# Optimization experiments

Measured on AMD Instinct MI355X. Metric: run time of the kernel, lower is better.

## Reference

```python
import jax, jax.numpy as jnp
import numpy as np

NUM_HEADS = 16
FIELD_SIZE = 512
SIGMA = 3.0
EMB = 1024


def _causal_kernel_fft(G, sigma):
    # kernel[i] = exp(-|i - G//2| / sigma) for i < G//2, else 0; normalized
    i = np.arange(G)
    dist = np.abs(i - G // 2)
    kernel = np.where(i >= G // 2, 0.0, np.exp(-dist / sigma)).astype(np.float32)
    kernel = kernel / (kernel.sum() + 1e-8)
    return jnp.asarray(np.fft.rfft(kernel), dtype=jnp.complex64)


def setup_inputs() -> dict:
    key = jax.random.key(0)
    ks = jax.random.split(key, 9)
    B, N, D = 4, 4096, EMB
    s = 1.0 / np.sqrt(D)
    return {
        "x": jax.random.normal(ks[0], (B, N, D), dtype=jnp.float32),
        "q_w": jax.random.uniform(ks[1], (D, D), minval=-s, maxval=s, dtype=jnp.float32),
        "q_b": jnp.zeros((D,), jnp.float32),
        "k_w": jax.random.uniform(ks[2], (D, D), minval=-s, maxval=s, dtype=jnp.float32),
        "k_b": jnp.zeros((D,), jnp.float32),
        "v_w": jax.random.uniform(ks[3], (D, D), minval=-s, maxval=s, dtype=jnp.float32),
        "v_b": jnp.zeros((D,), jnp.float32),
        "out_w": jax.random.uniform(ks[4], (D, D), minval=-s, maxval=s, dtype=jnp.float32),
        "out_b": jnp.zeros((D,), jnp.float32),
    }


def reference(x, q_w, q_b, k_w, k_b, v_w, v_b, out_w, out_b):
    B, N, D = x.shape
    H, hd, G = NUM_HEADS, D // NUM_HEADS, FIELD_SIZE

    # projections (q is computed in the original but unused downstream)
    q = x @ q_w.T + q_b  # noqa: F841 (faithful to original)
    k = (x @ k_w.T + k_b).reshape(B, N, H, hd).transpose(0, 2, 1, 3)  # (B,H,N,hd)
    v = (x @ v_w.T + v_b).reshape(B, N, H, hd).transpose(0, 2, 1, 3)

    # map sequence positions -> field bins (same for all b, h)
    pos = jnp.arange(N, dtype=jnp.float32) / max(N - 1, 1) * (G - 1)
    field_idx = jnp.clip(pos.astype(jnp.int32), 0, G - 1)  # (N,)

    # weighted values by key magnitude
    k_mag = jnp.linalg.norm(k, axis=-1, keepdims=True)  # (B,H,N,1)
    wv = v * k_mag  # (B,H,N,hd)

    # scatter-add tokens into field bins (vectorized over B,H,hd)
    field = jax.ops.segment_sum(wv.transpose(2, 0, 1, 3), field_idx,
                                num_segments=G)  # (G,B,H,hd)
    field = field.transpose(1, 2, 0, 3)  # (B,H,G,hd)

    # causal convolution along the field via FFT (circular, as in original)
    kfft = _causal_kernel_fft(G, SIGMA)
    f_fft = jnp.fft.rfft(field, n=G, axis=2)
    conv = jnp.fft.irfft(f_fft * kfft[None, None, :, None], n=G, axis=2)

    # gather back to token positions
    out = conv[:, :, field_idx, :]  # (B,H,N,hd)
    out = out.transpose(0, 2, 1, 3).reshape(B, N, D)
    return out @ out_w.T + out_b
```

## Files before the change

### kernel.cpp

```cpp
#include <hip/hip_runtime.h>
#include <hip/hip_bf16.h>

#define NPOS 4096
#define DIM  1024
#define GSZ  512

#define GAS __attribute__((address_space(1)))
#define LAS __attribute__((address_space(3)))

typedef __attribute__((ext_vector_type(8))) short bf16x8;
typedef __attribute__((ext_vector_type(4))) float f32x4;

__device__ __forceinline__ void async_load16(const void* g, void* l) {
  __builtin_amdgcn_global_load_lds((const GAS void*)g, (LAS void*)l, 16, 0, 0);
}

__device__ __forceinline__ int fidx_of(int n) {
  return (int)(((float)n / 4095.0f) * 511.0f);
}

__device__ __forceinline__ float bf2f(unsigned short s) {
  union { unsigned u; float f; } v; v.u = ((unsigned)s) << 16; return v.f;
}

__device__ __forceinline__ int bin_start(int g) {
  if (g >= GSZ) return NPOS;
  int i0 = (g * 4095 + 510) / 511;
  while (i0 > 0 && fidx_of(i0 - 1) >= g) --i0;
  while (i0 < NPOS && fidx_of(i0) < g) ++i0;
  return i0;
}

__device__ __forceinline__ void bin_range(int g, int& i0, int& i1) {
  i0 = bin_start(g);
  i1 = bin_start(g + 1);
}

__global__ __launch_bounds__(256) void cast_all(
    const float* __restrict__ x, const float* __restrict__ kw,
    const float* __restrict__ vw, const float* __restrict__ ow,
    __hip_bfloat16* __restrict__ xb, __hip_bfloat16* __restrict__ kvwb,
    __hip_bfloat16* __restrict__ outwb) {
  int blk = blockIdx.x;
  const float* src; __hip_bfloat16* dst; int off;
  if (blk < 8192)      { src = x;  dst = xb;              off = blk; }
  else if (blk < 8704) { src = kw; dst = kvwb;            off = blk - 8192; }
  else if (blk < 9216) { src = vw; dst = kvwb + 1048576;  off = blk - 8704; }
  else                 { src = ow; dst = outwb;           off = blk - 9216; }
  int i = (off * 256 + threadIdx.x) * 8;
  float4 f0 = *(const float4*)(src + i);
  float4 f1 = *(const float4*)(src + i + 4);
  ushort4 o0, o1;
  __hip_bfloat16 t;
  t = __float2bfloat16(f0.x); o0.x = *(unsigned short*)&t;
  t = __float2bfloat16(f0.y); o0.y = *(unsigned short*)&t;
  t = __float2bfloat16(f0.z); o0.z = *(unsigned short*)&t;
  t = __float2bfloat16(f0.w); o0.w = *(unsigned short*)&t;
  t = __float2bfloat16(f1.x); o1.x = *(unsigned short*)&t;
  t = __float2bfloat16(f1.y); o1.y = *(unsigned short*)&t;
  t = __float2bfloat16(f1.z); o1.z = *(unsigned short*)&t;
  t = __float2bfloat16(f1.w); o1.w = *(unsigned short*)&t;
  *(ushort4*)(dst + i) = o0;
  *(ushort4*)(dst + i + 4) = o1;
}


#define BAR()   __builtin_amdgcn_s_barrier()
#define LGKM0() do { asm volatile("s_waitcnt lgkmcnt(0)" ::: "memory"); \
                     __builtin_amdgcn_sched_barrier(0); } while (0)
#define VMW(N)  asm volatile("s_waitcnt vmcnt(" #N ")" ::: "memory")

#define STAGE_A(BUF, KT, C) \
  async_load16(ag0 + (size_t)(KT) * 64 + (size_t)(C) * 65536, &As[BUF][(C) * 4096 + ldst])
#define STAGE_B(BUF, KT, C) \
  async_load16(bg0 + (size_t)(KT) * 64 + (size_t)(C) * 65536, &Bs[BUF][(C) * 4096 + ldst])

#define STAGE_FULL(BUF, KT) do { \
    _Pragma("unroll") \
    for (int c_ = 0; c_ < 4; ++c_) { \
      STAGE_A(BUF, KT, c_); \
      STAGE_B(BUF, KT, c_); \
    } \
  } while (0)

#define LDA(BUF, MT, CB) (*(const bf16x8*)&As[BUF][abase + (MT) * 1024 + (CB)])
#define LDB(BUF, NT, CB) (*(const bf16x8*)&Bs[BUF][bbase + (NT) * 1024 + (CB)])

#define MFMA_Q(MQ, NQ, BF) do { \
    __builtin_amdgcn_s_setprio(1); \
    _Pragma("unroll") \
    for (int m_ = 0; m_ < 4; ++m_) { \
      _Pragma("unroll") \
      for (int n_ = 0; n_ < 2; ++n_) { \
        acc[(MQ)*4+m_][(NQ)*2+n_] = __builtin_amdgcn_mfma_f32_16x16x32_bf16( \
            af[m_][0], BF[n_][0], acc[(MQ)*4+m_][(NQ)*2+n_], 0, 0, 0); \
        acc[(MQ)*4+m_][(NQ)*2+n_] = __builtin_amdgcn_mfma_f32_16x16x32_bf16( \
            af[m_][1], BF[n_][1], acc[(MQ)*4+m_][(NQ)*2+n_], 0, 0, 0); \
      } \
    } \
    __builtin_amdgcn_s_setprio(0); \
  } while (0)

#define DO_TILE(BUF, KT) do { \
    const bool pf_ = (KT) + 2 < 16; \
     \
    _Pragma("unroll") \
    for (int m_ = 0; m_ < 4; ++m_) { af[m_][0] = LDA(BUF, m_, cb0); af[m_][1] = LDA(BUF, m_, cb1); } \
    _Pragma("unroll") \
    for (int n_ = 0; n_ < 2; ++n_) { b0f[n_][0] = LDB(BUF, n_, cb0); b0f[n_][1] = LDB(BUF, n_, cb1); } \
    BAR(); LGKM0(); \
    MFMA_Q(0, 0, b0f); \
    BAR(); \
     \
    _Pragma("unroll") \
    for (int n_ = 0; n_ < 2; ++n_) { b1f[n_][0] = LDB(BUF, 2 + n_, cb0); b1f[n_][1] = LDB(BUF, 2 + n_, cb1); } \
    if (pf_) { STAGE_A(BUF, (KT) + 2, 0); STAGE_A(BUF, (KT) + 2, 2); } \
    BAR(); LGKM0(); \
    MFMA_Q(0, 1, b1f); \
    BAR(); \
     \
    _Pragma("unroll") \
    for (int m_ = 0; m_ < 4; ++m_) { af[m_][0] = LDA(BUF, 4 + m_, cb0); af[m_][1] = LDA(BUF, 4 + m_, cb1); } \
    if (pf_) { STAGE_B(BUF, (KT) + 2, 0); STAGE_B(BUF, (KT) + 2, 1); \
               STAGE_B(BUF, (KT) + 2, 2); STAGE_B(BUF, (KT) + 2, 3); } \
    BAR(); LGKM0(); \
    MFMA_Q(1, 1, b1f); \
    BAR(); \
     \
    if (pf_) { STAGE_A(BUF, (KT) + 2, 1); STAGE_A(BUF, (KT) + 2, 3); } \
    MFMA_Q(1, 0, b0f); \
    if (pf_) { VMW(8); } else if ((KT) == 14) { VMW(0); } \
    BAR(); \
  } while (0)

__global__ __launch_bounds__(512, 2) void gemm_kv(
    const __hip_bfloat16* __restrict__ A,
    const __hip_bfloat16* __restrict__ B,
    const float* __restrict__ k_b, const float* __restrict__ v_b,
    __hip_bfloat16* __restrict__ Vb, float* __restrict__ knorm) {
  __shared__ __align__(16) __hip_bfloat16 As[2][16384];
  __shared__ __align__(16) __hip_bfloat16 Bs[2][16384];
  const int tid = threadIdx.x;

  const int l  = blockIdx.y * 64 + blockIdx.x;
  const int vv = (l & 7) * 64 + (l >> 3);
  const int bx = vv & 63, by = vv >> 6;
  const int bm = bx * 256;

  const int sb  = ((((tid & 7) * 16) ^ (((tid >> 3) & 7) << 4)) >> 1);
  const int r0  = tid >> 3;
  const __hip_bfloat16* ag0 = A + (size_t)(bm + r0) * 1024 + sb;
  const __hip_bfloat16* bg0 = B + (size_t)(by * 256 + r0) * 1024 + sb;
  const int ldst = tid * 8;

  const int wave = tid >> 6, lane = tid & 63;
  const int wr = wave >> 2, wc = wave & 3;
  const int m16 = lane & 15, quad = lane >> 4;
  const int swz  = (m16 & 7) << 4;
  const int cb0  = ((quad * 16)      ^ swz) >> 1;
  const int cb1  = ((quad * 16 + 64) ^ swz) >> 1;
  const int abase = wr * 8192 + m16 * 64;
  const int bbase = wc * 4096 + m16 * 64;

  f32x4 acc[8][4];
#pragma unroll
  for (int i = 0; i < 8; i++)
#pragma unroll
    for (int j2 = 0; j2 < 4; j2++) acc[i][j2] = (f32x4)0.f;

  bf16x8 af[4][2], b0f[2][2], b1f[2][2];

  STAGE_FULL(0, 0);
  STAGE_FULL(1, 1);
  VMW(8);
  BAR();

  for (int kt = 0; kt < 16; kt += 2) {
    DO_TILE(0, kt);
    DO_TILE(1, kt + 1);
  }

  if (by < 4) {
    const int head = by * 4 + wc;
    float bv[4];
#pragma unroll
    for (int nt = 0; nt < 4; nt++) bv[nt] = k_b[by * 256 + wc * 64 + nt * 16 + m16];
#pragma unroll
    for (int mt = 0; mt < 8; mt++) {
#pragma unroll
      for (int r = 0; r < 4; r++) {
        float s = 0.f;
#pragma unroll
        for (int nt = 0; nt < 4; nt++) {
          float t = acc[mt][nt][r] + bv[nt];
          s += t * t;
        }
        s += __shfl_xor(s, 1);
        s += __shfl_xor(s, 2);
        s += __shfl_xor(s, 4);
        s += __shfl_xor(s, 8);
        if (m16 == 0) {
          int row = bm + wr * 128 + mt * 16 + quad * 4 + r;
          knorm[(size_t)row * 16 + head] = sqrtf(s);
        }
      }
    }
  } else {
    const int colb = (by - 4) * 256 + wc * 64;
#pragma unroll
    for (int mt = 0; mt < 8; mt++) {
#pragma unroll
      for (int nt = 0; nt < 4; nt++) {
        int col = colb + nt * 16 + m16;
        float bvv = v_b[col];
#pragma unroll
        for (int r = 0; r < 4; r++) {
          int row = bm + wr * 128 + mt * 16 + quad * 4 + r;
          Vb[(size_t)row * 1024 + col] = __float2bfloat16(acc[mt][nt][r] + bvv);
        }
      }
    }
  }
}

__global__ __launch_bounds__(256) void gemm_outc(
    const __hip_bfloat16* __restrict__ A,
    const __hip_bfloat16* __restrict__ B,
    const float* __restrict__ bias,
    float* __restrict__ C) {
  const int K = 1024;
  __shared__ __align__(16) __hip_bfloat16 Aso[2][64 * 32];
  __shared__ __align__(16) __hip_bfloat16 Bso[2][64 * 32];
  __shared__ __align__(16) float ctile[64 * 68];
  const int tid = threadIdx.x;

  const int l   = blockIdx.y * 32 + blockIdx.x;
  const int xcd = l & 7, j = l >> 3;
  const int bx  = xcd * 4 + (j & 3);
  const int by  = j >> 2;
  const int bm = bx * 64, bn = by * 64;

  const int srow = tid >> 2;
  const int scol = (tid & 3) * 8;
  const __hip_bfloat16* ap = A + (size_t)(bm + srow) * K + scol;
  const __hip_bfloat16* bp = B + (size_t)(bn + srow) * K + scol;
  const int soff = srow * 32 + scol;

  const int wave = tid >> 6, lane = tid & 63;
  const int wm = (wave >> 1) * 32, wn = (wave & 1) * 32;
  const int m16 = lane & 15, quad = lane >> 4;

  f32x4 acc[2][2];
#pragma unroll
  for (int i = 0; i < 2; i++)
#pragma unroll
    for (int jj = 0; jj < 2; jj++) acc[i][jj] = (f32x4)0.f;

  for (int k0 = 0; k0 < K; k0 += 64) {
    async_load16(ap + k0,      &Aso[0][soff]);
    async_load16(bp + k0,      &Bso[0][soff]);
    async_load16(ap + k0 + 32, &Aso[1][soff]);
    async_load16(bp + k0 + 32, &Bso[1][soff]);
    __syncthreads();
#pragma unroll
    for (int h = 0; h < 2; h++) {
      bf16x8 afr[2], bfr[2];
#pragma unroll
      for (int mt = 0; mt < 2; mt++)
        afr[mt] = *(const bf16x8*)&Aso[h][(wm + mt * 16 + m16) * 32 + quad * 8];
#pragma unroll
      for (int nt = 0; nt < 2; nt++)
        bfr[nt] = *(const bf16x8*)&Bso[h][(wn + nt * 16 + m16) * 32 + quad * 8];
#pragma unroll
      for (int mt = 0; mt < 2; mt++)
#pragma unroll
        for (int nt = 0; nt < 2; nt++)
          acc[mt][nt] = __builtin_amdgcn_mfma_f32_16x16x32_bf16(afr[mt], bfr[nt], acc[mt][nt], 0, 0, 0);
    }
    __syncthreads();
  }

#pragma unroll
  for (int mt = 0; mt < 2; mt++) {
#pragma unroll
    for (int nt = 0; nt < 2; nt++) {
      int lcol = wn + nt * 16 + m16;
      float bv = bias[bn + lcol];
#pragma unroll
      for (int r = 0; r < 4; r++) {
        int lrow = wm + mt * 16 + quad * 4 + r;
        ctile[lrow * 68 + lcol] = acc[mt][nt][r] + bv;
      }
    }
  }
  __syncthreads();

  const int b  = bm >> 9;
  const int g0 = bm & (GSZ - 1);
  const int n0 = bin_start(g0);
  const int n1 = bin_start(g0 + 64);
  const int total = (n1 - n0) * 16;
  float* obase = C + (((size_t)b << 12)) * DIM + bn;
  for (int idx = tid; idx < total; idx += 256) {
    int n  = n0 + (idx >> 4);
    int c4 = (idx & 15) * 4;
    int lg = fidx_of(n) - g0;
    float4 v = *(const float4*)&ctile[lg * 68 + c4];
    *(float4*)(obase + (size_t)n * DIM + c4) = v;
  }
}

__global__ __launch_bounds__(256) void wv_field_kernel(
    const __hip_bfloat16* __restrict__ V, const float* __restrict__ knorm,
    float* __restrict__ field) {
  const int b = blockIdx.x, g = blockIdx.y;
  int i0, i1;
  bin_range(g, i0, i1);
  int cnt = i1 - i0;
  if (cnt > 9) cnt = 9;
  __shared__ float km[9][16];
  const int tid = threadIdx.x;
  if (tid < 144) {
    int r = tid >> 4, h = tid & 15;
    km[r][h] = (r < cnt) ? knorm[(size_t)(b * NPOS + i0 + r) * 16 + h] : 0.f;
  }
  __syncthreads();
  const int c0 = tid * 4, h = tid >> 4;
  const unsigned short* vbase = (const unsigned short*)V + (size_t)(b * NPOS + i0) * 1024 + c0;
  ushort4 vv[8];
  float ww[8];
#pragma unroll
  for (int j = 0; j < 8; ++j) {
    int jc = (j < cnt) ? j : 0;
    vv[j] = *(const ushort4*)(vbase + (size_t)jc * 1024);
    ww[j] = (j < cnt) ? km[j][h] : 0.f;
  }
  float a0 = 0.f, a1 = 0.f, a2 = 0.f, a3 = 0.f;
#pragma unroll
  for (int j = 0; j < 8; ++j) {
    a0 += ww[j] * bf2f(vv[j].x); a1 += ww[j] * bf2f(vv[j].y);
    a2 += ww[j] * bf2f(vv[j].z); a3 += ww[j] * bf2f(vv[j].w);
  }
  if (cnt == 9) {
    ushort4 v8 = *(const ushort4*)(vbase + (size_t)8 * 1024);
    float w8 = km[8][h];
    a0 += w8 * bf2f(v8.x); a1 += w8 * bf2f(v8.y);
    a2 += w8 * bf2f(v8.z); a3 += w8 * bf2f(v8.w);
  }
  *(float4*)(field + ((size_t)(b * GSZ + g)) * DIM + c0) = make_float4(a0, a1, a2, a3);
}

__global__ __launch_bounds__(256) void conv_ema_kernel(
    const float* __restrict__ field, __hip_bfloat16* __restrict__ convb) {
  const int b = blockIdx.x, h = blockIdx.y, n0 = blockIdx.z * 64;
  __shared__ float slab[128 * 64];
  const int tid = threadIdx.x;
  const float* fb = field + (size_t)b * GSZ * DIM + h * 64;
  for (int i = tid; i < 128 * 16; i += 256) {
    int row = i >> 4, c4 = i & 15;
    int gg = (n0 + 257 + row) & (GSZ - 1);
    *(float4*)&slab[row * 64 + c4 * 4] = *(const float4*)(fb + (size_t)gg * DIM + c4 * 4);
  }
  __syncthreads();
  const float a = 0.71653131057378927f;
  const float w1 = 1.0f - a;
  const int c = tid & 63, sub = tid >> 6;
  const int e0 = sub * 16;
  float acc = 0.f;
#pragma unroll 4
  for (int t = e0 + 79; t >= e0 + 16; --t)
    acc = w1 * slab[t * 64 + c] + a * acc;
#pragma unroll
  for (int t = e0 + 15; t >= e0; --t) {
    acc = w1 * slab[t * 64 + c] + a * acc;
    convb[((size_t)(b * GSZ) + n0 + t) * DIM + h * 64 + c] = __float2bfloat16(acc);
  }
}

extern "C" void kernel_launch(void* const* d_in, const int* in_sizes, int n_in,
                              void* d_out, int out_size, void* d_ws, size_t ws_size,
                              hipStream_t stream) {
  (void)in_sizes; (void)n_in; (void)out_size; (void)ws_size;
  const float* x     = (const float*)d_in[0];
  const float* k_w   = (const float*)d_in[3];
  const float* k_b   = (const float*)d_in[4];
  const float* v_w   = (const float*)d_in[5];
  const float* v_b   = (const float*)d_in[6];
  const float* out_w = (const float*)d_in[7];
  const float* out_b = (const float*)d_in[8];

  char* p = (char*)d_ws;
  __hip_bfloat16* xb    = (__hip_bfloat16*)p;         p += (size_t)16384 * 1024 * 2;
  __hip_bfloat16* kvwb  = (__hip_bfloat16*)p; p += (size_t)2048 * 1024 * 2;
  __hip_bfloat16* outwb = (__hip_bfloat16*)p; p += (size_t)1024 * 1024 * 2;
  __hip_bfloat16* Vb    = (__hip_bfloat16*)p; p += (size_t)16384 * 1024 * 2;
  float*          knorm = (float*)p;          p += (size_t)16384 * 16 * 4;
  float*          field = (float*)p;          p += (size_t)4 * 512 * 1024 * 4;
  __hip_bfloat16* convb = (__hip_bfloat16*)p;

  cast_all<<<9728, 256, 0, stream>>>(x, k_w, v_w, out_w, xb, kvwb, outwb);

  gemm_kv<<<dim3(64, 8), 512, 0, stream>>>(xb, kvwb, k_b, v_b, Vb, knorm);

  wv_field_kernel<<<dim3(4, 512), 256, 0, stream>>>(Vb, knorm, field);
  conv_ema_kernel<<<dim3(4, 16, 8), 256, 0, stream>>>(field, convb);

  gemm_outc<<<dim3(32, 16), 256, 0, stream>>>(convb, outwb, out_b, (float*)d_out);
}
```

Baseline: 246.4 us.

## Make gemm_kv blocks process two M tiles with continuous prefetch across tiles

Each gemm_kv workgroup now computes two consecutive 256-row output tiles, which halves the grid from 512 to 256 blocks. The async LDS prefetch pipeline runs across both tiles, so loads for the second tile overlap with the first tile's epilogue instead of paying a fresh pipeline fill. The cost is half as many blocks, which on a 256-CU part with two blocks per CU may leave CUs underused. It also makes each block's serial work longer.

```diff
diff --git a/kernel.cpp b/kernel.cpp
--- a/kernel.cpp
+++ b/kernel.cpp
@@ -70,16 +70,17 @@
                      __builtin_amdgcn_sched_barrier(0); } while (0)
 #define VMW(N)  asm volatile("s_waitcnt vmcnt(" #N ")" ::: "memory")
 
-#define STAGE_A(BUF, KT, C) \
-  async_load16(ag0 + (size_t)(KT) * 64 + (size_t)(C) * 65536, &As[BUF][(C) * 4096 + ldst])
-#define STAGE_B(BUF, KT, C) \
-  async_load16(bg0 + (size_t)(KT) * 64 + (size_t)(C) * 65536, &Bs[BUF][(C) * 4096 + ldst])
-
-#define STAGE_FULL(BUF, KT) do { \
+#define STAGE_A2(BUF, T2, C) \
+  async_load16((((T2) < 16) ? ag0a : ag0b) + (size_t)((T2) & 15) * 64 + (size_t)(C) * 65536, \
+               &As[BUF][(C) * 4096 + ldst])
+#define STAGE_B2(BUF, T2, C) \
+  async_load16(bg0 + (size_t)((T2) & 15) * 64 + (size_t)(C) * 65536, &Bs[BUF][(C) * 4096 + ldst])
+
+#define STAGE_FULL(BUF, T2) do { \
     _Pragma("unroll") \
     for (int c_ = 0; c_ < 4; ++c_) { \
-      STAGE_A(BUF, KT, c_); \
-      STAGE_B(BUF, KT, c_); \
+      STAGE_A2(BUF, T2, c_); \
+      STAGE_B2(BUF, T2, c_); \
     } \
   } while (0)
 
@@ -102,7 +103,7 @@
   } while (0)
 
 #define DO_TILE(BUF, KT) do { \
-    const bool pf_ = (KT) + 2 < 16; \
+    const bool pf_ = (KT) + 2 < 32; \
      \
     _Pragma("unroll") \
     for (int m_ = 0; m_ < 4; ++m_) { af[m_][0] = LDA(BUF, m_, cb0); af[m_][1] = LDA(BUF, m_, cb1); } \
@@ -114,24 +115,68 @@
      \
     _Pragma("unroll") \
     for (int n_ = 0; n_ < 2; ++n_) { b1f[n_][0] = LDB(BUF, 2 + n_, cb0); b1f[n_][1] = LDB(BUF, 2 + n_, cb1); } \
-    if (pf_) { STAGE_A(BUF, (KT) + 2, 0); STAGE_A(BUF, (KT) + 2, 2); } \
+    if (pf_) { STAGE_A2(BUF, (KT) + 2, 0); STAGE_A2(BUF, (KT) + 2, 2); } \
     BAR(); LGKM0(); \
     MFMA_Q(0, 1, b1f); \
     BAR(); \
      \
     _Pragma("unroll") \
     for (int m_ = 0; m_ < 4; ++m_) { af[m_][0] = LDA(BUF, 4 + m_, cb0); af[m_][1] = LDA(BUF, 4 + m_, cb1); } \
-    if (pf_) { STAGE_B(BUF, (KT) + 2, 0); STAGE_B(BUF, (KT) + 2, 1); \
-               STAGE_B(BUF, (KT) + 2, 2); STAGE_B(BUF, (KT) + 2, 3); } \
+    if (pf_) { STAGE_B2(BUF, (KT) + 2, 0); STAGE_B2(BUF, (KT) + 2, 1); \
+               STAGE_B2(BUF, (KT) + 2, 2); STAGE_B2(BUF, (KT) + 2, 3); } \
     BAR(); LGKM0(); \
     MFMA_Q(1, 1, b1f); \
     BAR(); \
      \
-    if (pf_) { STAGE_A(BUF, (KT) + 2, 1); STAGE_A(BUF, (KT) + 2, 3); } \
+    if (pf_) { STAGE_A2(BUF, (KT) + 2, 1); STAGE_A2(BUF, (KT) + 2, 3); } \
     MFMA_Q(1, 0, b0f); \
-    if (pf_) { VMW(8); } else if ((KT) == 14) { VMW(0); } \
+    if (pf_) { VMW(8); } else if ((KT) == 30) { VMW(0); } \
     BAR(); \
   } while (0)
+
+#define EPILOGUE(BM) do { \
+  if (by < 4) { \
+    const int head = by * 4 + wc; \
+    float bv[4]; \
+    _Pragma("unroll") \
+    for (int nt = 0; nt < 4; nt++) bv[nt] = k_b[by * 256 + wc * 64 + nt * 16 + m16]; \
+    _Pragma("unroll") \
+    for (int mt = 0; mt < 8; mt++) { \
+      _Pragma("unroll") \
+      for (int r = 0; r < 4; r++) { \
+        float s = 0.f; \
+        _Pragma("unroll") \
+        for (int nt = 0; nt < 4; nt++) { \
+          float t_ = acc[mt][nt][r] + bv[nt]; \
+          s += t_ * t_; \
+        } \
+        s += __shfl_xor(s, 1); \
+        s += __shfl_xor(s, 2); \
+        s += __shfl_xor(s, 4); \
+        s += __shfl_xor(s, 8); \
+        if (m16 == 0) { \
+          int row = (BM) + wr * 128 + mt * 16 + quad * 4 + r; \
+          knorm[(size_t)row * 16 + head] = sqrtf(s); \
+        } \
+      } \
+    } \
+  } else { \
+    const int colb = (by - 4) * 256 + wc * 64; \
+    _Pragma("unroll") \
+    for (int mt = 0; mt < 8; mt++) { \
+      _Pragma("unroll") \
+      for (int nt = 0; nt < 4; nt++) { \
+        int col = colb + nt * 16 + m16; \
+        float bvv = v_b[col]; \
+        _Pragma("unroll") \
+        for (int r = 0; r < 4; r++) { \
+          int row = (BM) + wr * 128 + mt * 16 + quad * 4 + r; \
+          Vb[(size_t)row * 1024 + col] = __float2bfloat16(acc[mt][nt][r] + bvv); \
+        } \
+      } \
+    } \
+  } \
+} while (0)
 
 __global__ __launch_bounds__(512, 2) void gemm_kv(
     const __hip_bfloat16* __restrict__ A,
@@ -142,15 +187,16 @@
   __shared__ __align__(16) __hip_bfloat16 Bs[2][16384];
   const int tid = threadIdx.x;
 
-  const int l  = blockIdx.y * 64 + blockIdx.x;
-  const int vv = (l & 7) * 64 + (l >> 3);
-  const int bx = vv & 63, by = vv >> 6;
-  const int bm = bx * 256;
+  const int l  = blockIdx.y * 32 + blockIdx.x;
+  const int vv = (l & 7) * 32 + (l >> 3);
+  const int i  = vv & 31, by = vv >> 5;
+  const int bm1 = i * 512, bm2 = bm1 + 256;
 
   const int sb  = ((((tid & 7) * 16) ^ (((tid >> 3) & 7) << 4)) >> 1);
   const int r0  = tid >> 3;
-  const __hip_bfloat16* ag0 = A + (size_t)(bm + r0) * 1024 + sb;
-  const __hip_bfloat16* bg0 = B + (size_t)(by * 256 + r0) * 1024 + sb;
+  const __hip_bfloat16* ag0a = A + (size_t)(bm1 + r0) * 1024 + sb;
+  const __hip_bfloat16* ag0b = A + (size_t)(bm2 + r0) * 1024 + sb;
+  const __hip_bfloat16* bg0  = B + (size_t)(by * 256 + r0) * 1024 + sb;
   const int ldst = tid * 8;
 
   const int wave = tid >> 6, lane = tid & 63;
@@ -164,9 +210,9 @@
 
   f32x4 acc[8][4];
 #pragma unroll
-  for (int i = 0; i < 8; i++)
-#pragma unroll
-    for (int j2 = 0; j2 < 4; j2++) acc[i][j2] = (f32x4)0.f;
+  for (int ii = 0; ii < 8; ii++)
+#pragma unroll
+    for (int j2 = 0; j2 < 4; j2++) acc[ii][j2] = (f32x4)0.f;
 
   bf16x8 af[4][2], b0f[2][2], b1f[2][2];
 
@@ -175,52 +221,19 @@
   VMW(8);
   BAR();
 
-  for (int kt = 0; kt < 16; kt += 2) {
-    DO_TILE(0, kt);
-    DO_TILE(1, kt + 1);
-  }
-
-  if (by < 4) {
-    const int head = by * 4 + wc;
-    float bv[4];
-#pragma unroll
-    for (int nt = 0; nt < 4; nt++) bv[nt] = k_b[by * 256 + wc * 64 + nt * 16 + m16];
-#pragma unroll
-    for (int mt = 0; mt < 8; mt++) {
-#pragma unroll
-      for (int r = 0; r < 4; r++) {
-        float s = 0.f;
-#pragma unroll
-        for (int nt = 0; nt < 4; nt++) {
-          float t = acc[mt][nt][r] + bv[nt];
-          s += t * t;
-        }
-        s += __shfl_xor(s, 1);
-        s += __shfl_xor(s, 2);
-        s += __shfl_xor(s, 4);
-        s += __shfl_xor(s, 8);
-        if (m16 == 0) {
-          int row = bm + wr * 128 + mt * 16 + quad * 4 + r;
-          knorm[(size_t)row * 16 + head] = sqrtf(s);
-        }
-      }
+  for (int t = 0; t < 32; t += 2) {
+    DO_TILE(0, t);
+    DO_TILE(1, t + 1);
+    if (t == 14) {
+      EPILOGUE(bm1);
+#pragma unroll
+      for (int ii = 0; ii < 8; ii++)
+#pragma unroll
+        for (int j2 = 0; j2 < 4; j2++) acc[ii][j2] = (f32x4)0.f;
     }
-  } else {
-    const int colb = (by - 4) * 256 + wc * 64;
-#pragma unroll
-    for (int mt = 0; mt < 8; mt++) {
-#pragma unroll
-      for (int nt = 0; nt < 4; nt++) {
-        int col = colb + nt * 16 + m16;
-        float bvv = v_b[col];
-#pragma unroll
-        for (int r = 0; r < 4; r++) {
-          int row = bm + wr * 128 + mt * 16 + quad * 4 + r;
-          Vb[(size_t)row * 1024 + col] = __float2bfloat16(acc[mt][nt][r] + bvv);
-        }
-      }
-    }
-  }
+  }
+
+  EPILOGUE(bm2);
 }
 
 __global__ __launch_bounds__(256) void gemm_outc(
@@ -400,7 +413,7 @@
 
   cast_all<<<9728, 256, 0, stream>>>(x, k_w, v_w, out_w, xb, kvwb, outwb);
 
-  gemm_kv<<<dim3(64, 8), 512, 0, stream>>>(xb, kvwb, k_b, v_b, Vb, knorm);
+  gemm_kv<<<dim3(32, 8), 512, 0, stream>>>(xb, kvwb, k_b, v_b, Vb, knorm);
 
   wv_field_kernel<<<dim3(4, 512), 256, 0, stream>>>(Vb, knorm, field);
   conv_ema_kernel<<<dim3(4, 16, 8), 256, 0, stream>>>(field, convb);
```

Measured after the change: 294.8 us. +19.6%, slower.
